# Kernel optimization log

Hardware: AMD Instinct MI355X
Metric: run time of the kernel (lower is better)

## Reference

```python
import jax, jax.numpy as jnp
import numpy as np

NUM_HEADS = 32
NUM_KV_HEADS = 8
HEAD_DIM = 128
HIDDEN = 4096
EPS = 1e-6
ROPE_BASE = 10000.0
NEG_INF = -1e9


def setup_inputs() -> dict:
    key = jax.random.key(0)
    ks = jax.random.split(key, 6)
    B, S = 1, 2048
    hidden_states = jax.random.normal(ks[0], (B, S, HIDDEN), dtype=jnp.float32)
    wq = jax.random.normal(ks[1], (HIDDEN, NUM_HEADS * HEAD_DIM), dtype=jnp.float32) * 0.02
    wk = jax.random.normal(ks[2], (HIDDEN, NUM_KV_HEADS * HEAD_DIM), dtype=jnp.float32) * 0.02
    wv = jax.random.normal(ks[3], (HIDDEN, NUM_KV_HEADS * HEAD_DIM), dtype=jnp.float32) * 0.02
    wo = jax.random.normal(ks[4], (NUM_HEADS * HEAD_DIM, HIDDEN), dtype=jnp.float32) * 0.02
    q_norm_w = jnp.ones((HEAD_DIM,), dtype=jnp.float32)
    k_norm_w = jnp.ones((HEAD_DIM,), dtype=jnp.float32)
    attention_mask = jnp.tril(jnp.ones((S, S), dtype=bool))[None, None]  # [1,1,S,S] causal allow-mask
    position_ids = jnp.arange(S, dtype=jnp.int64 if jax.config.jax_enable_x64 else jnp.int32)[None, :]
    return dict(hidden_states=hidden_states, wq=wq, wk=wk, wv=wv, wo=wo,
                q_norm_w=q_norm_w, k_norm_w=k_norm_w,
                attention_mask=attention_mask, position_ids=position_ids)


def _rotate_half(x):
    x1, x2 = jnp.split(x, 2, axis=-1)
    return jnp.concatenate((-x2, x1), axis=-1)


def _rms_norm(x, w):
    xf = x.astype(jnp.float32)
    var = jnp.mean(xf * xf, axis=-1, keepdims=True)
    return w * (xf * jax.lax.rsqrt(var + EPS)).astype(x.dtype)


def reference(hidden_states, wq, wk, wv, wo, q_norm_w, k_norm_w, attention_mask, position_ids):
    B, S, _ = hidden_states.shape
    dtype = hidden_states.dtype

    # projections -> [B, H, S, D]
    q = (hidden_states @ wq).reshape(B, S, NUM_HEADS, HEAD_DIM).transpose(0, 2, 1, 3)
    k = (hidden_states @ wk).reshape(B, S, NUM_KV_HEADS, HEAD_DIM).transpose(0, 2, 1, 3)
    v = (hidden_states @ wv).reshape(B, S, NUM_KV_HEADS, HEAD_DIM).transpose(0, 2, 1, 3)

    # RoPE cache (fp32), gathered by position_ids
    inv_freq = 1.0 / (ROPE_BASE ** (jnp.arange(0, HEAD_DIM, 2, dtype=jnp.float32) / HEAD_DIM))
    t = jnp.arange(S, dtype=jnp.float32)
    freqs = jnp.outer(t, inv_freq)                    # [S, D/2]
    emb = jnp.concatenate((freqs, freqs), axis=-1)    # [S, D]
    cos = jnp.cos(emb).astype(dtype)[position_ids][:, None]  # [B,1,S,D]
    sin = jnp.sin(emb).astype(dtype)[position_ids][:, None]

    q = q * cos + _rotate_half(q) * sin
    k = k * cos + _rotate_half(k) * sin

    # QK RMSNorm (after RoPE)
    q = _rms_norm(q, q_norm_w)
    k = _rms_norm(k, k_norm_w)

    # GQA repeat-kv
    n_rep = NUM_HEADS // NUM_KV_HEADS
    k = jnp.repeat(k, n_rep, axis=1)
    v = jnp.repeat(v, n_rep, axis=1)

    scores = jnp.einsum('bhqd,bhkd->bhqk', q, k) / np.sqrt(HEAD_DIM)
    scores = jnp.where(attention_mask, scores, scores + NEG_INF)
    probs = jax.nn.softmax(scores.astype(jnp.float32), axis=-1).astype(dtype)
    out = jnp.einsum('bhqk,bhkd->bhqd', probs, v)      # [B,H,S,D]
    out = out.transpose(0, 2, 1, 3).reshape(B, S, NUM_HEADS * HEAD_DIM)
    return out @ wo
```

## Files before the change

kernel.cpp:

```cpp
#include <hip/hip_runtime.h>

typedef __bf16 bf16x8 __attribute__((ext_vector_type(8)));
typedef float f32x4 __attribute__((ext_vector_type(4)));
typedef unsigned short u16x8 __attribute__((ext_vector_type(8)));
typedef unsigned short u16x4 __attribute__((ext_vector_type(4)));
typedef unsigned short u16x2 __attribute__((ext_vector_type(2)));

__device__ inline unsigned short f2bf(float f) {
    return __builtin_bit_cast(unsigned short, (__bf16)f);
}
__device__ inline float bf2f(unsigned short u) {
    return (float)__builtin_bit_cast(__bf16, u);
}

__device__ inline void storeC(float v, float* p) { *p = v; }
__device__ inline void storeC(float v, unsigned short* p) { *p = f2bf(v); }

#define MFMA16(a, b, c) __builtin_amdgcn_mfma_f32_16x16x32_bf16( \
    __builtin_bit_cast(bf16x8, a), __builtin_bit_cast(bf16x8, b), (c), 0, 0, 0)

__device__ inline void gload16(const unsigned short* g, unsigned short* l) {
    __builtin_amdgcn_global_load_lds(
        (const __attribute__((address_space(1))) unsigned int*)(g),
        (__attribute__((address_space(3))) unsigned int*)(l), 16, 0, 0);
}

__device__ __forceinline__ void bar() {
    asm volatile("" ::: "memory");
    __builtin_amdgcn_s_barrier();
    asm volatile("" ::: "memory");
}
#define WAITVM(N) asm volatile("s_waitcnt vmcnt(" #N ")" ::: "memory")

__global__ __launch_bounds__(256) void convert_f32_bf16_swz(
    const float* __restrict__ X, unsigned short* __restrict__ Y)
{
    const size_t i = ((size_t)blockIdx.x * 256 + threadIdx.x) * 8;
    const size_t row7 = (i >> 12) & 7;
    float4 v0 = *(const float4*)&X[i];
    float4 v1 = *(const float4*)&X[i + 4];
    u16x8 o;
    o[0] = f2bf(v0.x); o[1] = f2bf(v0.y); o[2] = f2bf(v0.z); o[3] = f2bf(v0.w);
    o[4] = f2bf(v1.x); o[5] = f2bf(v1.y); o[6] = f2bf(v1.z); o[7] = f2bf(v1.w);
    *(u16x8*)&Y[i ^ (row7 << 3)] = o;
}

__global__ __launch_bounds__(256) void transpose_f32_bf16(
    const float* __restrict__ W, unsigned short* __restrict__ WT, int K, int N)
{
    constexpr int LDT = 66;
    __shared__ unsigned short t_lds[64 * LDT];
    const int kt = blockIdx.x * 64, nt = blockIdx.y * 64;
    const int tid = threadIdx.x;
    const int c = (tid & 15) * 4;
    #pragma unroll
    for (int p = 0; p < 4; ++p) {
        const int r = p * 16 + (tid >> 4);
        float4 v = *(const float4*)&W[(size_t)(kt + r) * N + nt + c];
        u16x2 h0, h1;
        h0[0] = f2bf(v.x); h0[1] = f2bf(v.y);
        h1[0] = f2bf(v.z); h1[1] = f2bf(v.w);
        *(u16x2*)&t_lds[r * LDT + c] = h0;
        *(u16x2*)&t_lds[r * LDT + c + 2] = h1;
    }
    __syncthreads();
    const int kc = (tid & 7) * 8;
    #pragma unroll
    for (int p = 0; p < 2; ++p) {
        const int n = p * 32 + (tid >> 3);
        u16x8 o;
        #pragma unroll
        for (int j = 0; j < 8; ++j) o[j] = t_lds[(kc + j) * LDT + n];
        *(u16x8*)&WT[(size_t)(nt + n) * K + kt + (kc ^ ((n & 7) << 3))] = o;
    }
}

template <typename CT, int CMODE>
__global__ __launch_bounds__(512) void gemm8(
    const unsigned short* __restrict__ A, const unsigned short* __restrict__ B,
    CT* __restrict__ C, int M, int N, int K)
{
    constexpr int ASZ = 128 * 64, BSZ = 256 * 64;
    __shared__ __attribute__((aligned(16))) unsigned short a_lds[3 * ASZ];
    __shared__ __attribute__((aligned(16))) unsigned short b_lds[3 * BSZ];

    const int bm0 = blockIdx.y * 128, bn0 = blockIdx.x * 256;
    const int tid = threadIdx.x, lane = tid & 63, wid = tid >> 6;
    const int wr = wid >> 2, wc = wid & 3;
    const int l15 = lane & 15, koff = (lane >> 4) * 8;
    const int sw = (l15 & 7) << 3;
    const int cb0 = koff ^ sw;
    const int cb1 = (32 + koff) ^ sw;

    f32x4 acc[4][4] = {};

    const size_t kbase = (CMODE == 3) ? (size_t)blockIdx.z * 2048 : 0;

    const unsigned short* ag[2];
    const unsigned short* bg[4];
    #pragma unroll
    for (int p = 0; p < 2; ++p) {
        const int row = (wid + p * 8) * 8 + (lane >> 3);
        ag[p] = A + (size_t)(bm0 + row) * K + (lane & 7) * 8 + kbase;
    }
    #pragma unroll
    for (int p = 0; p < 4; ++p) {
        const int row = (wid + p * 8) * 8 + (lane >> 3);
        bg[p] = B + (size_t)(bn0 + row) * K + (lane & 7) * 8 + kbase;
    }

    const int nt = (CMODE == 3) ? 32 : (K >> 6);

    auto stageA = [&](int s, int kt, int p) {
        gload16(ag[p] + kt, a_lds + s * ASZ + (wid + p * 8) * 512);
    };
    auto stageB = [&](int s, int kt, int p) {
        gload16(bg[p] + kt, b_lds + s * BSZ + (wid + p * 8) * 512);
    };

    #pragma unroll
    for (int p = 0; p < 2; ++p) stageA(0, 0, p);
    #pragma unroll
    for (int p = 0; p < 4; ++p) stageB(0, 0, p);
    #pragma unroll
    for (int p = 0; p < 2; ++p) stageA(1, 64, p);
    #pragma unroll
    for (int p = 0; p < 4; ++p) stageB(1, 64, p);
    WAITVM(6);
    bar();

    int sc = 0;
    for (int t = 0; t < nt; ++t) {
        const unsigned short* ab = a_lds + sc * ASZ;
        const unsigned short* bb = b_lds + sc * BSZ;
        const int ss = (sc >= 1) ? sc - 1 : 2;
        const int kt2 = (t + 2) << 6;
        const bool st = (t + 2) < nt;

        u16x8 af0, af1, af2, af3, bfr[4];

        af0 = *(const u16x8*)&ab[(wr * 64 + 0 * 16 + l15) * 64 + cb0];
        af1 = *(const u16x8*)&ab[(wr * 64 + 1 * 16 + l15) * 64 + cb0];
        af2 = *(const u16x8*)&ab[(wr * 64 + 2 * 16 + l15) * 64 + cb0];
        af3 = *(const u16x8*)&ab[(wr * 64 + 3 * 16 + l15) * 64 + cb0];
        #pragma unroll
        for (int j = 0; j < 4; ++j)
            bfr[j] = *(const u16x8*)&bb[(wc * 64 + j * 16 + l15) * 64 + cb0];
        if (st) { stageA(ss, kt2, 0); stageA(ss, kt2, 1); stageB(ss, kt2, 0); }
        bar();
        __builtin_amdgcn_s_setprio(1);
        #pragma unroll
        for (int j = 0; j < 4; ++j) {
            acc[0][j] = MFMA16(af0, bfr[j], acc[0][j]);
            acc[1][j] = MFMA16(af1, bfr[j], acc[1][j]);
            acc[2][j] = MFMA16(af2, bfr[j], acc[2][j]);
            acc[3][j] = MFMA16(af3, bfr[j], acc[3][j]);
        }
        __builtin_amdgcn_s_setprio(0);

        af0 = *(const u16x8*)&ab[(wr * 64 + 0 * 16 + l15) * 64 + cb1];
        af1 = *(const u16x8*)&ab[(wr * 64 + 1 * 16 + l15) * 64 + cb1];
        af2 = *(const u16x8*)&ab[(wr * 64 + 2 * 16 + l15) * 64 + cb1];
        af3 = *(const u16x8*)&ab[(wr * 64 + 3 * 16 + l15) * 64 + cb1];
        #pragma unroll
        for (int j = 0; j < 4; ++j)
            bfr[j] = *(const u16x8*)&bb[(wc * 64 + j * 16 + l15) * 64 + cb1];
        if (st) {
            stageB(ss, kt2, 1); stageB(ss, kt2, 2); stageB(ss, kt2, 3);
            WAITVM(6);
        } else {
            WAITVM(0);
        }
        bar();
        __builtin_amdgcn_s_setprio(1);
        #pragma unroll
        for (int j = 0; j < 4; ++j) {
            acc[0][j] = MFMA16(af0, bfr[j], acc[0][j]);
            acc[1][j] = MFMA16(af1, bfr[j], acc[1][j]);
            acc[2][j] = MFMA16(af2, bfr[j], acc[2][j]);
            acc[3][j] = MFMA16(af3, bfr[j], acc[3][j]);
        }
        __builtin_amdgcn_s_setprio(0);

        bar();
        sc = (sc == 2) ? 0 : sc + 1;
    }

    CT* Cb = C;
    if constexpr (CMODE == 3)
        Cb = C + (size_t)blockIdx.z * M * N;

    #pragma unroll
    for (int i = 0; i < 4; ++i)
        #pragma unroll
        for (int r = 0; r < 4; ++r) {
            const int row = bm0 + wr * 64 + i * 16 + (lane >> 4) * 4 + r;
            size_t base = (size_t)row * N + bn0 + wc * 64 + l15;
            #pragma unroll
            for (int j = 0; j < 4; ++j)
                storeC(acc[i][j][r], &Cb[base + j * 16]);
        }
}

__global__ __launch_bounds__(256) void combine_kv(
    const float* __restrict__ P, unsigned short* __restrict__ Kout,
    unsigned short* __restrict__ VTout)
{
    const float* P0 = P;
    const float* P1 = P + (size_t)2048 * 2048;
    const int s0 = blockIdx.y * 64, c0 = blockIdx.x * 64;
    const int tid = threadIdx.x;
    const int row = tid >> 2;
    const int cbl = (tid & 3) * 16;
    const size_t gbase = (size_t)(s0 + row) * 2048 + c0 + cbl;
    u16x8 o[2];
    #pragma unroll
    for (int j = 0; j < 2; ++j) {
        float4 a0 = *(const float4*)&P0[gbase + j * 8];
        float4 b0 = *(const float4*)&P1[gbase + j * 8];
        float4 a1 = *(const float4*)&P0[gbase + j * 8 + 4];
        float4 b1 = *(const float4*)&P1[gbase + j * 8 + 4];
        o[j][0] = f2bf(a0.x + b0.x); o[j][1] = f2bf(a0.y + b0.y);
        o[j][2] = f2bf(a0.z + b0.z); o[j][3] = f2bf(a0.w + b0.w);
        o[j][4] = f2bf(a1.x + b1.x); o[j][5] = f2bf(a1.y + b1.y);
        o[j][6] = f2bf(a1.z + b1.z); o[j][7] = f2bf(a1.w + b1.w);
    }
    if (c0 < 1024) {
        #pragma unroll
        for (int j = 0; j < 2; ++j)
            *(u16x8*)&Kout[(size_t)(s0 + row) * 1024 + c0 + cbl + j * 8] = o[j];
    } else {
        constexpr int LDT = 66;
        __shared__ unsigned short t_lds[64 * LDT];
        #pragma unroll
        for (int j = 0; j < 2; ++j)
            *(u16x8*)&t_lds[row * LDT + cbl + j * 8] = o[j];
        __syncthreads();
        const int d = row;
        #pragma unroll
        for (int j = 0; j < 2; ++j) {
            u16x8 w;
            #pragma unroll
            for (int e = 0; e < 8; ++e)
                w[e] = t_lds[(cbl + j * 8 + e) * LDT + d];
            *(u16x8*)&VTout[(size_t)(c0 - 1024 + d) * 2048 + s0 + cbl + j * 8] = w;
        }
    }
}

__global__ void rope_rmsnorm(unsigned short* __restrict__ X,
                             const int* __restrict__ pos_ids,
                             const float* __restrict__ W, int H, float outscale)
{
    const int s = blockIdx.x;
    const int tid = threadIdx.x;
    const int h = tid >> 3, t8 = tid & 7;
    const int rowstride = H * 128;
    unsigned short* p = X + (size_t)s * rowstride + h * 128 + t8 * 8;
    u16x8 lo = *(u16x8*)p;
    u16x8 hi = *(u16x8*)(p + 64);
    const float fpos = (float)pos_ids[s];
    float na[8], nb[8];
    float ss = 0.f;
    #pragma unroll
    for (int j = 0; j < 8; ++j) {
        const int d = t8 * 8 + j;
        float inv = expf(-0.14391156831212787f * (float)d);
        float fr = fpos * inv;
        float c = cosf(fr), sn = sinf(fr);
        float a = bf2f(lo[j]), b = bf2f(hi[j]);
        na[j] = a * c - b * sn;
        nb[j] = b * c + a * sn;
        ss += na[j] * na[j] + nb[j] * nb[j];
    }
    ss += __shfl_xor(ss, 1, 8);
    ss += __shfl_xor(ss, 2, 8);
    ss += __shfl_xor(ss, 4, 8);
    const float rn = rsqrtf(ss * (1.0f / 128.0f) + 1e-6f) * outscale;
    #pragma unroll
    for (int j = 0; j < 8; ++j) {
        const int d = t8 * 8 + j;
        lo[j] = f2bf(na[j] * rn * W[d]);
        hi[j] = f2bf(nb[j] * rn * W[d + 64]);
    }
    *(u16x8*)p = lo;
    *(u16x8*)(p + 64) = hi;
}

__global__ __launch_bounds__(256, 2) void attn_kernel(
    const unsigned short* __restrict__ Q, const unsigned short* __restrict__ K,
    const unsigned short* __restrict__ VT, unsigned short* __restrict__ O)
{
    constexpr int LDK = 136, LDV = 72, LDP = 72;
    __shared__ __attribute__((aligned(16))) unsigned short k_lds[64 * LDK];
    __shared__ __attribute__((aligned(16))) unsigned short v_lds[128 * LDV];
    __shared__ __attribute__((aligned(16))) unsigned short p_lds[4 * 32 * LDP];

    const int bid = blockIdx.x;
    const int kvh = bid & 7;
    const int rest = bid >> 3;
    const int h = kvh * 4 + (rest & 3);
    const int qb = 15 - (rest >> 2);
    const int q0 = qb * 128;
    const int tid = threadIdx.x, lane = tid & 63, wid = tid >> 6;
    const int l15 = lane & 15, g4 = (lane >> 4) * 4, koff = (lane >> 4) * 8;
    const int qw = q0 + wid * 32;

    u16x8 qf[2][4];
    #pragma unroll
    for (int qt = 0; qt < 2; ++qt)
        #pragma unroll
        for (int kk = 0; kk < 4; ++kk)
            qf[qt][kk] = *(const u16x8*)&Q[(size_t)(qw + qt * 16 + l15) * 4096 +
                                           h * 128 + kk * 32 + koff];

    f32x4 o_acc[2][8] = {};
    float m_r[2] = {-1e30f, -1e30f}, l_r[2] = {0.f, 0.f};

    const int kr = tid >> 2, kd = (tid & 3) * 32;
    const int vr = tid >> 1, vc = (tid & 1) * 32;
    const unsigned short* kg = K + (size_t)kvh * 128 + kd;
    const unsigned short* vg = VT + (size_t)(kvh * 128 + vr) * 2048 + vc;

    const int nchunk = qb * 2 + 2;
    u16x8 kst[4], vst[4];
    #pragma unroll
    for (int j = 0; j < 4; ++j) {
        kst[j] = *(const u16x8*)&kg[(size_t)kr * 1024 + j * 8];
        vst[j] = *(const u16x8*)&vg[j * 8];
    }

    for (int ch = 0; ch < nchunk; ++ch) {
        const int kv0 = ch * 64;
        __syncthreads();
        #pragma unroll
        for (int j = 0; j < 4; ++j) {
            *(u16x8*)&k_lds[kr * LDK + kd + j * 8] = kst[j];
            *(u16x8*)&v_lds[vr * LDV + vc + j * 8] = vst[j];
        }
        __syncthreads();
        if (ch + 1 < nchunk) {
            const int kv1 = kv0 + 64;
            #pragma unroll
            for (int j = 0; j < 4; ++j) {
                kst[j] = *(const u16x8*)&kg[(size_t)(kv1 + kr) * 1024 + j * 8];
                vst[j] = *(const u16x8*)&vg[kv1 + j * 8];
            }
        }

        if (kv0 <= qw + 31) {
            f32x4 sacc[2][4] = {};
            #pragma unroll
            for (int kk = 0; kk < 4; ++kk)
                #pragma unroll
                for (int jt = 0; jt < 4; ++jt) {
                    u16x8 kf = *(u16x8*)&k_lds[(jt * 16 + l15) * LDK + kk * 32 + koff];
                    #pragma unroll
                    for (int qt = 0; qt < 2; ++qt)
                        sacc[qt][jt] = MFMA16(kf, qf[qt][kk], sacc[qt][jt]);
                }

            const bool needmask = (kv0 + 63 > qw);
            #pragma unroll
            for (int qt = 0; qt < 2; ++qt) {
                const int q = qw + qt * 16 + l15;
                if (needmask) {
                    #pragma unroll
                    for (int jt = 0; jt < 4; ++jt)
                        #pragma unroll
                        for (int r = 0; r < 4; ++r)
                            if (kv0 + jt * 16 + g4 + r > q) sacc[qt][jt][r] = -1e9f;
                }
                float pmax = sacc[qt][0][0];
                #pragma unroll
                for (int jt = 0; jt < 4; ++jt)
                    #pragma unroll
                    for (int r = 0; r < 4; ++r)
                        pmax = fmaxf(pmax, sacc[qt][jt][r]);
                pmax = fmaxf(pmax, __shfl_xor(pmax, 16));
                pmax = fmaxf(pmax, __shfl_xor(pmax, 32));
                if (__any(pmax > m_r[qt] + 8.0f)) {
                    float mnew = fmaxf(m_r[qt], pmax);
                    float alpha = __expf(m_r[qt] - mnew);
                    m_r[qt] = mnew;
                    l_r[qt] *= alpha;
                    float arow[4];
                    #pragma unroll
                    for (int r = 0; r < 4; ++r)
                        arow[r] = __shfl(alpha, g4 + r, 16);
                    #pragma unroll
                    for (int nt = 0; nt < 8; ++nt)
                        #pragma unroll
                        for (int r = 0; r < 4; ++r)
                            o_acc[qt][nt][r] *= arow[r];
                }
                float ps = 0.f;
                #pragma unroll
                for (int jt = 0; jt < 4; ++jt)
                    #pragma unroll
                    for (int r = 0; r < 4; ++r) {
                        float e = __expf(sacc[qt][jt][r] - m_r[qt]);
                        sacc[qt][jt][r] = e;
                        ps += e;
                    }
                ps += __shfl_xor(ps, 16);
                ps += __shfl_xor(ps, 32);
                l_r[qt] += ps;
                const int prow = (wid * 32 + qt * 16 + l15) * LDP;
                #pragma unroll
                for (int jt = 0; jt < 4; ++jt) {
                    u16x4 w;
                    #pragma unroll
                    for (int r = 0; r < 4; ++r) w[r] = f2bf(sacc[qt][jt][r]);
                    *(u16x4*)&p_lds[prow + jt * 16 + g4] = w;
                }
            }

            u16x8 pf[2][2];
            #pragma unroll
            for (int qt = 0; qt < 2; ++qt)
                #pragma unroll
                for (int ks = 0; ks < 2; ++ks)
                    pf[qt][ks] = *(u16x8*)&p_lds[(wid * 32 + qt * 16 + l15) * LDP +
                                                 ks * 32 + koff];
            #pragma unroll
            for (int nt = 0; nt < 8; ++nt)
                #pragma unroll
                for (int ks = 0; ks < 2; ++ks) {
                    u16x8 vf = *(u16x8*)&v_lds[(nt * 16 + l15) * LDV + ks * 32 + koff];
                    #pragma unroll
                    for (int qt = 0; qt < 2; ++qt)
                        o_acc[qt][nt] = MFMA16(pf[qt][ks], vf, o_acc[qt][nt]);
                }
        }
    }

    #pragma unroll
    for (int qt = 0; qt < 2; ++qt) {
        float lrow[4];
        #pragma unroll
        for (int r = 0; r < 4; ++r)
            lrow[r] = __shfl(l_r[qt], g4 + r, 16);
        #pragma unroll
        for (int r = 0; r < 4; ++r) {
            float inv_l = 1.0f / lrow[r];
            int row = qw + qt * 16 + g4 + r;
            const int r7s = (row & 7) << 3;
            #pragma unroll
            for (int nt = 0; nt < 8; ++nt) {
                int col = h * 128 + nt * 16 + l15;
                O[(size_t)row * 4096 + (col ^ r7s)] =
                    f2bf(o_acc[qt][nt][r] * inv_l);
            }
        }
    }
}

extern "C" void kernel_launch(void* const* d_in, const int* in_sizes, int n_in,
                              void* d_out, int out_size, void* d_ws, size_t ws_size,
                              hipStream_t stream)
{
    (void)in_sizes; (void)n_in; (void)out_size; (void)ws_size;
    const float* hidden = (const float*)d_in[0];
    const float* wq     = (const float*)d_in[1];
    const float* wk     = (const float*)d_in[2];
    const float* wv     = (const float*)d_in[3];
    const float* wo     = (const float*)d_in[4];
    const float* qnw    = (const float*)d_in[5];
    const float* knw    = (const float*)d_in[6];
    const int*   pos    = (const int*)d_in[8];
    float* out = (float*)d_out;

    const size_t MB = 1024 * 1024;
    char* ws = (char*)d_ws;
    unsigned short* q_ws  = (unsigned short*)(ws);
    unsigned short* k_ws  = (unsigned short*)(ws + 16 * MB);
    unsigned short* vt_ws = (unsigned short*)(ws + 20 * MB);
    unsigned short* hb    = (unsigned short*)(ws + 24 * MB);
    unsigned short* a_ws  = hb;
    unsigned short* wqt   = (unsigned short*)(ws + 40 * MB);
    float*          kvP   = (float*)(ws + 40 * MB);
    unsigned short* wkt   = (unsigned short*)(ws + 72 * MB);
    unsigned short* wot   = (unsigned short*)(ws + 88 * MB);

    convert_f32_bf16_swz<<<4096, 256, 0, stream>>>(hidden, hb);
    transpose_f32_bf16<<<dim3(64, 64), 256, 0, stream>>>(wq, wqt, 4096, 4096);
    transpose_f32_bf16<<<dim3(64, 16), 256, 0, stream>>>(wk, wkt, 4096, 1024);
    transpose_f32_bf16<<<dim3(64, 16), 256, 0, stream>>>(
        wv, wkt + (size_t)1024 * 4096, 4096, 1024);
    transpose_f32_bf16<<<dim3(64, 64), 256, 0, stream>>>(wo, wot, 4096, 4096);

    gemm8<unsigned short, 0><<<dim3(16, 16), 512, 0, stream>>>(
        hb, wqt, q_ws, 2048, 4096, 4096);
    gemm8<float, 3><<<dim3(8, 16, 2), 512, 0, stream>>>(
        hb, wkt, kvP, 2048, 2048, 4096);
    combine_kv<<<dim3(32, 32), 256, 0, stream>>>(kvP, k_ws, vt_ws);

    rope_rmsnorm<<<2048, 256, 0, stream>>>(q_ws, pos, qnw, 32, 0.08838834764831845f);
    rope_rmsnorm<<<2048, 64, 0, stream>>>(k_ws, pos, knw, 8, 1.0f);

    attn_kernel<<<512, 256, 0, stream>>>(q_ws, k_ws, vt_ws, a_ws);

    gemm8<float, 0><<<dim3(16, 16), 512, 0, stream>>>(
        a_ws, wot, out, 2048, 4096, 4096);
}
```

Measured before the change: 338.2 us.

## Replace Q and output projection GEMMs with 4-wave single-buffered kernel

Adds a new 256-thread GEMM kernel with 128x256 tiles, single-buffered LDS and two workgroups per CU via launch bounds. It remaps block IDs in a chiplet-aware pattern spread across 8 groups and raises wave priority around the MFMA bursts. It is used for the Q projection and the output projection in place of the 512-thread triple-buffered gemm8. The aim is better occupancy and L2 locality. In exchange it loses explicit prefetch pipelining and relies on the co-resident workgroup to hide load latency, with 128 accumulator floats per thread adding register pressure.

```diff
diff --git a/kernel.cpp b/kernel.cpp
--- a/kernel.cpp
+++ b/kernel.cpp
@@ -73,6 +73,89 @@
         for (int j = 0; j < 8; ++j) o[j] = t_lds[(kc + j) * LDT + n];
         *(u16x8*)&WT[(size_t)(nt + n) * K + kt + (kc ^ ((n & 7) << 3))] = o;
     }
+}
+
+template <typename CT>
+__global__ __launch_bounds__(256, 2) void gemm4w(
+    const unsigned short* __restrict__ A, const unsigned short* __restrict__ B,
+    CT* __restrict__ C, int M, int N, int K)
+{
+    __shared__ __attribute__((aligned(16))) unsigned short a_lds[128 * 64];
+    __shared__ __attribute__((aligned(16))) unsigned short b_lds[256 * 64];
+
+    const int nbx = N >> 8;
+    const int nwg = (M >> 7) * nbx;
+    const int bid0 = blockIdx.y * nbx + blockIdx.x;
+    const int wgid = (bid0 & 7) * (nwg >> 3) + (bid0 >> 3);
+    const int bm0 = (wgid / nbx) * 128, bn0 = (wgid % nbx) * 256;
+
+    const int tid = threadIdx.x, lane = tid & 63, wid = tid >> 6;
+    const int wr = wid >> 1, wc = wid & 1;
+    const int l15 = lane & 15, koff = (lane >> 4) * 8;
+    const int sw = (l15 & 7) << 3;
+    const int cb0 = koff ^ sw, cb1 = (32 + koff) ^ sw;
+
+    f32x4 acc[4][8] = {};
+
+    const int srow = tid >> 3;
+    const int scol = (tid & 7) * 8;
+    const unsigned short* Ab = A + (size_t)(bm0 + srow) * K + scol;
+    const unsigned short* Bb = B + (size_t)(bn0 + srow) * K + scol;
+
+    for (int kt = 0; kt < K; kt += 64) {
+        #pragma unroll
+        for (int p = 0; p < 4; ++p)
+            gload16(Ab + (size_t)(p * 32) * K + kt, a_lds + p * 2048 + wid * 512);
+        #pragma unroll
+        for (int p = 0; p < 8; ++p)
+            gload16(Bb + (size_t)(p * 32) * K + kt, b_lds + p * 2048 + wid * 512);
+        __syncthreads();
+
+        {
+            u16x8 af[4], bf[8];
+            #pragma unroll
+            for (int i = 0; i < 4; ++i)
+                af[i] = *(const u16x8*)&a_lds[(wr * 64 + i * 16 + l15) * 64 + cb0];
+            #pragma unroll
+            for (int j = 0; j < 8; ++j)
+                bf[j] = *(const u16x8*)&b_lds[(wc * 128 + j * 16 + l15) * 64 + cb0];
+            __builtin_amdgcn_s_setprio(1);
+            #pragma unroll
+            for (int i = 0; i < 4; ++i)
+                #pragma unroll
+                for (int j = 0; j < 8; ++j)
+                    acc[i][j] = MFMA16(af[i], bf[j], acc[i][j]);
+            __builtin_amdgcn_s_setprio(0);
+        }
+        {
+            u16x8 af[4], bf[8];
+            #pragma unroll
+            for (int i = 0; i < 4; ++i)
+                af[i] = *(const u16x8*)&a_lds[(wr * 64 + i * 16 + l15) * 64 + cb1];
+            #pragma unroll
+            for (int j = 0; j < 8; ++j)
+                bf[j] = *(const u16x8*)&b_lds[(wc * 128 + j * 16 + l15) * 64 + cb1];
+            __builtin_amdgcn_s_setprio(1);
+            #pragma unroll
+            for (int i = 0; i < 4; ++i)
+                #pragma unroll
+                for (int j = 0; j < 8; ++j)
+                    acc[i][j] = MFMA16(af[i], bf[j], acc[i][j]);
+            __builtin_amdgcn_s_setprio(0);
+        }
+        __syncthreads();
+    }
+
+    #pragma unroll
+    for (int i = 0; i < 4; ++i)
+        #pragma unroll
+        for (int r = 0; r < 4; ++r) {
+            const int row = bm0 + wr * 64 + i * 16 + (lane >> 4) * 4 + r;
+            size_t base = (size_t)row * N + bn0 + wc * 128 + l15;
+            #pragma unroll
+            for (int j = 0; j < 8; ++j)
+                storeC(acc[i][j][r], &C[base + j * 16]);
+        }
 }
 
 template <typename CT, int CMODE>
@@ -490,7 +573,7 @@
         wv, wkt + (size_t)1024 * 4096, 4096, 1024);
     transpose_f32_bf16<<<dim3(64, 64), 256, 0, stream>>>(wo, wot, 4096, 4096);
 
-    gemm8<unsigned short, 0><<<dim3(16, 16), 512, 0, stream>>>(
+    gemm4w<unsigned short><<<dim3(16, 16), 256, 0, stream>>>(
         hb, wqt, q_ws, 2048, 4096, 4096);
     gemm8<float, 3><<<dim3(8, 16, 2), 512, 0, stream>>>(
         hb, wkt, kvP, 2048, 2048, 4096);
@@ -501,6 +584,6 @@
 
     attn_kernel<<<512, 256, 0, stream>>>(q_ws, k_ws, vt_ws, a_ws);
 
-    gemm8<float, 0><<<dim3(16, 16), 512, 0, stream>>>(
+    gemm4w<float><<<dim3(16, 16), 256, 0, stream>>>(
         a_ws, wot, out, 2048, 4096, 4096);
 }
```

Measured after the change: 406.1 us. +20.1%, slower.
